# Kernel optimization log

Measured on AMD Instinct MI355X. Metric: run time of the kernel, lower is better.

The kernel has to match this reference:

```python
import jax, jax.numpy as jnp
import numpy as np

L = 2          # num_layers
D = 2048       # embed_dim
HQ = 16        # num_q_heads
HK = 4         # num_kv_heads
HD = D // HQ   # head_size = 128
G = HQ // HK   # q_to_kv_ratio = 4
P = 8192       # embed_dim_proj
V = 32000      # vocab_size
B = 1
S = 2048
EPS = 1e-5
THETA = 500000.0
NEG = -1e30


def setup_inputs() -> dict:
    key = jax.random.key(0)
    ks = jax.random.split(key, 8)
    s = 0.02
    return {
        "tokens": jax.random.randint(ks[0], (B, S), 0, V, dtype=jnp.int32),
        "embed": jax.random.normal(ks[1], (V, D), jnp.float32) * s,
        "attn_norm_w": jnp.ones((L, D), jnp.float32),
        "qkv_w": jax.random.normal(ks[2], (L, D, D + 2 * HK * HD), jnp.float32) * s,
        "attn_out_w": jax.random.normal(ks[3], (L, D, D), jnp.float32) * s,
        "mlp_norm_w": jnp.ones((L, D), jnp.float32),
        "mlp_in_w": jax.random.normal(ks[4], (L, D, 2 * P), jnp.float32) * s,
        "mlp_out_w": jax.random.normal(ks[5], (L, P, D), jnp.float32) * s,
        "final_norm_w": jnp.ones((D,), jnp.float32),
        "lm_head_w": jax.random.normal(ks[6], (D, V), jnp.float32) * s,
    }


def _rms(x, w):
    return w * (x * jax.lax.rsqrt(jnp.mean(x * x, axis=-1, keepdims=True) + EPS))


def _rope_cos_sin():
    inv = 1.0 / (THETA ** (jnp.arange(0, HD, 2, dtype=jnp.float32) / HD))  # [HD/2]
    ang = jnp.arange(S, dtype=jnp.float32)[:, None] * inv[None, :]         # [S, HD/2]
    return jnp.cos(ang), jnp.sin(ang)


def _rope(t, cos, sin):
    # t: [B,S,H,HD]; interleaved complex rotation on (even, odd) pairs
    x = t.reshape(t.shape[:-1] + (HD // 2, 2))
    x0, x1 = x[..., 0], x[..., 1]
    c = cos[None, :, None, :]
    sn = sin[None, :, None, :]
    out = jnp.stack([x0 * c - x1 * sn, x0 * sn + x1 * c], axis=-1)
    return out.reshape(t.shape)


def _layer(x, nw1, wqkv, wo, nw2, wi, wmo, cos, sin, mask):
    # attention block (pre-norm, residual)
    h = _rms(x, nw1)
    qkv = h @ wqkv
    q = qkv[..., :D].reshape(B, S, HQ, HD)
    k = qkv[..., D:D + HK * HD].reshape(B, S, HK, HD)
    v = qkv[..., D + HK * HD:].reshape(B, S, HK, HD)
    q = _rope(q, cos, sin)
    k = _rope(k, cos, sin)
    # GQA: repeat_interleave along head dim
    k = jnp.repeat(k, G, axis=2)
    v = jnp.repeat(v, G, axis=2)
    scores = jnp.einsum('bqhd,bkhd->bhqk', q, k) / np.float32(np.sqrt(HD))
    scores = jnp.where(mask, scores, NEG)
    attn = jax.nn.softmax(scores, axis=-1)
    o = jnp.einsum('bhqk,bkhd->bqhd', attn, v).reshape(B, S, D)
    x = x + o @ wo
    # SwiGLU block (pre-norm, residual)
    h = _rms(x, nw2)
    gu = h @ wi
    gate, up = gu[..., :P], gu[..., P:]
    x = x + (jax.nn.silu(gate) * up) @ wmo
    return x


def reference(tokens, embed, attn_norm_w, qkv_w, attn_out_w, mlp_norm_w,
              mlp_in_w, mlp_out_w, final_norm_w, lm_head_w):
    cos, sin = _rope_cos_sin()
    mask = jnp.tril(jnp.ones((S, S), dtype=bool))  # offset=0 prefill -> causal
    x = embed[tokens]  # [B,S,D]
    for i in range(L):
        x = _layer(x, attn_norm_w[i], qkv_w[i], attn_out_w[i],
                   mlp_norm_w[i], mlp_in_w[i], mlp_out_w[i], cos, sin, mask)
    return _rms(x, final_norm_w) @ lm_head_w  # [B,S,V]
```

## Files before the change

### kernel.cpp

```cpp
#include <hip/hip_runtime.h>
#include <math.h>

#define S_LEN 2048
#define DMODEL 2048
#define NHQ 16
#define NHK 4
#define HDIM 128
#define PDIM 8192
#define VOCAB 32000
#define NQKV 3072
#define EPSI 1e-5f

typedef unsigned short u16;
typedef unsigned int u32;
typedef __bf16 bf16x8 __attribute__((ext_vector_type(8)));
typedef float f32x4 __attribute__((ext_vector_type(4)));

__device__ __forceinline__ u16 f2bf(float f){
  u32 u = __builtin_bit_cast(u32, f);
  u += 0x7fffu + ((u >> 16) & 1u);
  return (u16)(u >> 16);
}
__device__ __forceinline__ float bf2f(u16 h){
  u32 u = ((u32)h) << 16;
  return __builtin_bit_cast(float, u);
}
__device__ __forceinline__ bf16x8 ld8(const u16* p){
  return __builtin_bit_cast(bf16x8, *(const uint4*)p);
}
__device__ __forceinline__ f32x4 mfma16(bf16x8 a, bf16x8 b, f32x4 c){
  return __builtin_amdgcn_mfma_f32_16x16x32_bf16(a, b, c, 0, 0, 0);
}

#define GLOAD_LDS16(gp, lp) __builtin_amdgcn_global_load_lds( \
    (__attribute__((address_space(1))) void*)(gp), \
    (__attribute__((address_space(3))) void*)(lp), 16, 0, 0)

__device__ __forceinline__ bf16x8 lds_frag(const u16* Lb, int R, int g){
  const int Rp = R >> 1;
  const int s8 = (((R & 1) << 2) | g) ^ (Rp & 7);
  return ld8(Lb + Rp * 64 + s8 * 8);
}
__device__ __forceinline__ void stage_sw(const u16* base, long row0, int K, int kt,
                                         int q, u16* Ldst_waveuniform){
  const int Rp = q >> 3;
  const int u = (q & 7) ^ (Rp & 7);
  const int R = (Rp << 1) | (u >> 2);
  const u16* gp = base + (row0 + R) * (long)K + kt + ((u & 3) << 3);
  GLOAD_LDS16(gp, Ldst_waveuniform);
}

__global__ void k_embed(const int* __restrict__ tok, const float* __restrict__ emb,
                        float* __restrict__ x){
  const int s = blockIdx.x, t = threadIdx.x;
  const long r = tok[s];
  const float4* src = (const float4*)(emb + r * DMODEL);
  float4* dst = (float4*)(x + (long)s * DMODEL);
  dst[t] = src[t];
  dst[t + 256] = src[t + 256];
}

__global__ void k_rmsnorm(const float* __restrict__ x, const float* __restrict__ w,
                          u16* __restrict__ out){
  const int s = blockIdx.x, t = threadIdx.x;
  const float4* xr = (const float4*)(x + (long)s * DMODEL);
  const float4 a = xr[t], b = xr[t + 256];
  float ss = a.x*a.x + a.y*a.y + a.z*a.z + a.w*a.w
           + b.x*b.x + b.y*b.y + b.z*b.z + b.w*b.w;
  #pragma unroll
  for (int off = 32; off > 0; off >>= 1) ss += __shfl_down(ss, off, 64);
  __shared__ float part[4];
  if ((t & 63) == 0) part[t >> 6] = ss;
  __syncthreads();
  const float r = rsqrtf((part[0] + part[1] + part[2] + part[3]) * (1.f / 2048.f) + EPSI);
  const float4* wr = (const float4*)w;
  const float4 wa = wr[t], wb = wr[t + 256];
  uint2 ua, ub;
  ua.x = (u32)f2bf(a.x*r*wa.x) | ((u32)f2bf(a.y*r*wa.y) << 16);
  ua.y = (u32)f2bf(a.z*r*wa.z) | ((u32)f2bf(a.w*r*wa.w) << 16);
  ub.x = (u32)f2bf(b.x*r*wb.x) | ((u32)f2bf(b.y*r*wb.y) << 16);
  ub.y = (u32)f2bf(b.z*r*wb.z) | ((u32)f2bf(b.w*r*wb.w) << 16);
  *(uint2*)(out + (long)s * DMODEL + 4 * t) = ua;
  *(uint2*)(out + (long)s * DMODEL + 1024 + 4 * t) = ub;
}

__global__ __launch_bounds__(256) void k_convT(const float* __restrict__ W,
                                               u16* __restrict__ Wt, int N, int K){
  const int n0 = blockIdx.x * 64, k0 = blockIdx.y * 64;
  const int t = threadIdx.x;
  __shared__ u16 T[64][72];
  const int r = t >> 4, c = (t & 15) << 2;
  #pragma unroll
  for (int p = 0; p < 4; ++p){
    const int k = p * 16 + r;
    const float4 v = *(const float4*)(W + (long)(k0 + k) * N + n0 + c);
    T[c + 0][k] = f2bf(v.x);
    T[c + 1][k] = f2bf(v.y);
    T[c + 2][k] = f2bf(v.z);
    T[c + 3][k] = f2bf(v.w);
  }
  __syncthreads();
  const int nr = t >> 3, kc = (t & 7) << 3;
  #pragma unroll
  for (int p = 0; p < 2; ++p){
    const int n = p * 32 + nr;
    *(uint4*)(Wt + (long)(n0 + n) * K + k0 + kc) = *(const uint4*)(&T[n][kc]);
  }
}

template<int OUT_BF16, int RES>
__global__ __launch_bounds__(256) void k_gemm(const u16* __restrict__ A, const u16* __restrict__ Bt,
                                              void* C, const float* Rs,
                                              int M, int N, int K){
  const int bm = blockIdx.x, bn = blockIdx.y;
  const int t = threadIdx.x;
  const int w = t >> 6, lane = t & 63, l15 = lane & 15, g = lane >> 4;
  const int wr = w >> 1, wc = w & 1;
  __shared__ u16 As[4096];
  __shared__ u16 Bs[4096];
  f32x4 acc[4][4] = {};
  const long arow = (long)bm * 128;
  const long brow = (long)bn * 128;
  for (int kt = 0; kt < K; kt += 32){
    __syncthreads();
    #pragma unroll
    for (int c = 0; c < 2; ++c){
      const int q0 = ((w << 1) | c) << 6;
      const int q  = q0 | lane;
      stage_sw(A,  arow, K, kt, q, As + q0 * 8);
      stage_sw(Bt, brow, K, kt, q, Bs + q0 * 8);
    }
    __syncthreads();
    bf16x8 af[4], bfr[4];
    #pragma unroll
    for (int i = 0; i < 4; ++i)
      af[i] = lds_frag(As, wr * 64 + i * 16 + l15, g);
    #pragma unroll
    for (int i = 0; i < 4; ++i)
      bfr[i] = lds_frag(Bs, wc * 64 + i * 16 + l15, g);
    #pragma unroll
    for (int mi = 0; mi < 4; ++mi)
      #pragma unroll
      for (int ni = 0; ni < 4; ++ni)
        acc[mi][ni] = mfma16(af[mi], bfr[ni], acc[mi][ni]);
  }
  const int row0 = bm * 128 + wr * 64, col0 = bn * 128 + wc * 64;
  #pragma unroll
  for (int mi = 0; mi < 4; ++mi){
    #pragma unroll
    for (int ni = 0; ni < 4; ++ni){
      #pragma unroll
      for (int r = 0; r < 4; ++r){
        const long ri = row0 + mi * 16 + g * 4 + r;
        const long ci = col0 + ni * 16 + l15;
        float v = acc[mi][ni][r];
        if (RES) v += Rs[ri * N + ci];
        if (OUT_BF16) ((u16*)C)[ri * N + ci] = f2bf(v);
        else          ((float*)C)[ri * N + ci] = v;
      }
    }
  }
}

template<int OUT_BF16>
__global__ __launch_bounds__(512, 2) void k_gemm256(const u16* __restrict__ A,
                                                    const u16* __restrict__ Bt,
                                                    void* C, int M, int N, int K){
  __shared__ u16 L[65536];
  const int t = threadIdx.x;
  const int w = t >> 6, lane = t & 63, l15 = lane & 15, g = lane >> 4;
  const int wr = w >> 2, wc = w & 3;
  const int nbm = M >> 8;
  int id = blockIdx.x;
  {
    const int cpx = gridDim.x >> 3;
    id = (id & 7) * cpx + (id >> 3);
  }
  const int bm = id % nbm, bn = id / nbm;
  const int NT = K >> 5;

  const int Rp0 = t >> 3;
  const int u0  = (t & 7) ^ (Rp0 & 7);
  const int R0  = (Rp0 << 1) | (u0 >> 2);
  const u16* pA0 = A  + ((long)bm * 256 + R0) * (long)K + ((u0 & 3) << 3);
  const u16* pB0 = Bt + ((long)bn * 256 + R0) * (long)K + ((u0 & 3) << 3);
  const u16* pA1 = pA0 + (long)128 * K;
  const u16* pB1 = pB0 + (long)128 * K;
  const int w0 = (t & ~63) * 8;

  auto stagef = [&](int slot){
    u16* ldsA = L + slot * 8192;
    u16* ldsB = L + 32768 + slot * 8192;
    GLOAD_LDS16(pA0, ldsA + w0);
    GLOAD_LDS16(pB0, ldsB + w0);
    GLOAD_LDS16(pA1, ldsA + 4096 + w0);
    GLOAD_LDS16(pB1, ldsB + 4096 + w0);
    pA0 += 32; pB0 += 32; pA1 += 32; pB1 += 32;
  };

  stagef(0); stagef(1); stagef(2);
  asm volatile("s_waitcnt vmcnt(8)" ::: "memory");
  __builtin_amdgcn_s_barrier();

  f32x4 acc[8][4] = {};
  for (int tt = 0; tt < NT; ++tt){
    const u16* sA = L + (tt & 3) * 8192;
    const u16* sB = L + 32768 + (tt & 3) * 8192;
    bf16x8 af[8], bfr[4];
    #pragma unroll
    for (int j = 0; j < 8; ++j)
      af[j] = lds_frag(sA, wr * 128 + j * 16 + l15, g);
    #pragma unroll
    for (int n = 0; n < 4; ++n)
      bfr[n] = lds_frag(sB, wc * 64 + n * 16 + l15, g);
    if (tt + 3 < NT) stagef((tt + 3) & 3);
    if (tt + 1 < NT){
      asm volatile("s_waitcnt lgkmcnt(0)" ::: "memory");
      if (tt + 3 < NT)      asm volatile("s_waitcnt vmcnt(8)" ::: "memory");
      else if (tt + 2 < NT) asm volatile("s_waitcnt vmcnt(4)" ::: "memory");
      else                  asm volatile("s_waitcnt vmcnt(0)" ::: "memory");
      __builtin_amdgcn_s_barrier();
    }
    __builtin_amdgcn_s_setprio(1);
    #pragma unroll
    for (int mi = 0; mi < 8; ++mi)
      #pragma unroll
      for (int ni = 0; ni < 4; ++ni)
        acc[mi][ni] = mfma16(af[mi], bfr[ni], acc[mi][ni]);
    __builtin_amdgcn_s_setprio(0);
  }
  const int row0 = bm * 256 + wr * 128, col0 = bn * 256 + wc * 64;
  #pragma unroll
  for (int mi = 0; mi < 8; ++mi){
    #pragma unroll
    for (int ni = 0; ni < 4; ++ni){
      #pragma unroll
      for (int r = 0; r < 4; ++r){
        const long ri = row0 + mi * 16 + g * 4 + r;
        const long ci = col0 + ni * 16 + l15;
        const float v = acc[mi][ni][r];
        if (OUT_BF16) ((u16*)C)[ri * N + ci] = f2bf(v);
        else          ((float*)C)[ri * N + ci] = v;
      }
    }
  }
}

__global__ void k_rope(u16* __restrict__ qkv){
  const int idx = blockIdx.x * 256 + threadIdx.x;
  const int i = idx & 63;
  const int head = (idx >> 6) % 20;
  const int s = idx / (64 * 20);
  const long base = (long)s * NQKV + (head < NHQ ? head * HDIM : DMODEL + (head - NHQ) * HDIM);
  u32* p = (u32*)(qkv + base + 2 * i);
  const u32 v = *p;
  const float x0 = bf2f((u16)(v & 0xffffu)), x1 = bf2f((u16)(v >> 16));
  const float ang = (float)s * exp2f(-0.29580575889569023f * (float)i);
  float sn, cs;
  sincosf(ang, &sn, &cs);
  const float y0 = x0 * cs - x1 * sn;
  const float y1 = x0 * sn + x1 * cs;
  *p = (u32)f2bf(y0) | ((u32)f2bf(y1) << 16);
}

__global__ __launch_bounds__(256) void k_attn(const u16* __restrict__ qkv, u16* __restrict__ o){
  const int qb = blockIdx.x, h = blockIdx.y;
  const int kh = h >> 2;
  const int t = threadIdx.x, w = t >> 6, lane = t & 63, l15 = lane & 15, g = lane >> 4;
  __shared__ u16 Ks[64 * 144];
  __shared__ u16 Vt[128 * 80];
  __shared__ u16 Ps[4][16 * 72];
  const int q0 = qb * 64 + w * 16;
  bf16x8 aq[4];
  #pragma unroll
  for (int d0 = 0; d0 < 4; ++d0)
    aq[d0] = ld8(qkv + (long)(q0 + l15) * NQKV + h * HDIM + d0 * 32 + g * 8);
  f32x4 acc_o[8] = {};
  float mst[4], lst[4];
  #pragma unroll
  for (int r = 0; r < 4; ++r){ mst[r] = -1e30f; lst[r] = 0.f; }
  const float scale = 0.08838834764831843f;
  const int krow = t >> 2, kc0 = (t & 3) << 5;
  const int vkv = (t & 31) << 1, vd0 = (t >> 5) << 4;
  for (int kt = 0; kt <= qb; ++kt){
    const int kv0 = kt << 6;
    __syncthreads();
    {
      const u16* kp = qkv + (long)(kv0 + krow) * NQKV + DMODEL + kh * HDIM + kc0;
      u16* kd = Ks + krow * 144 + kc0;
      #pragma unroll
      for (int c = 0; c < 4; ++c)
        *(uint4*)(kd + c * 8) = *(const uint4*)(kp + c * 8);
    }
    {
      const u16* vp = qkv + (long)(kv0 + vkv) * NQKV + DMODEL + 512 + kh * HDIM + vd0;
      const uint4 a0 = *(const uint4*)vp;
      const uint4 a1 = *(const uint4*)(vp + 8);
      const uint4 b0 = *(const uint4*)(vp + NQKV);
      const uint4 b1 = *(const uint4*)(vp + NQKV + 8);
      const u32 aw[8] = {a0.x,a0.y,a0.z,a0.w,a1.x,a1.y,a1.z,a1.w};
      const u32 bw[8] = {b0.x,b0.y,b0.z,b0.w,b1.x,b1.y,b1.z,b1.w};
      #pragma unroll
      for (int i2 = 0; i2 < 8; ++i2){
        *(u32*)(Vt + (vd0 + 2 * i2)     * 80 + vkv) = (aw[i2] & 0xffffu) | ((bw[i2] & 0xffffu) << 16);
        *(u32*)(Vt + (vd0 + 2 * i2 + 1) * 80 + vkv) = (aw[i2] >> 16)     | ((bw[i2] >> 16) << 16);
      }
    }
    __syncthreads();
    f32x4 sacc[4] = {};
    #pragma unroll
    for (int d0 = 0; d0 < 4; ++d0){
      #pragma unroll
      for (int j = 0; j < 4; ++j){
        const bf16x8 bk = ld8(Ks + (j * 16 + l15) * 144 + d0 * 32 + g * 8);
        sacc[j] = mfma16(aq[d0], bk, sacc[j]);
      }
    }
    float p[4][4], scl[4];
    #pragma unroll
    for (int r = 0; r < 4; ++r){
      const int qrow = q0 + g * 4 + r;
      float mx = -1e30f;
      #pragma unroll
      for (int j = 0; j < 4; ++j){
        float sv = sacc[j][r] * scale;
        sv = (kv0 + j * 16 + l15 <= qrow) ? sv : -1e30f;
        p[j][r] = sv;
        mx = fmaxf(mx, sv);
      }
      #pragma unroll
      for (int off = 1; off < 16; off <<= 1) mx = fmaxf(mx, __shfl_xor(mx, off, 64));
      const float mnew = fmaxf(mst[r], mx);
      scl[r] = __expf(mst[r] - mnew);
      float rs = 0.f;
      #pragma unroll
      for (int j = 0; j < 4; ++j){ p[j][r] = __expf(p[j][r] - mnew); rs += p[j][r]; }
      #pragma unroll
      for (int off = 1; off < 16; off <<= 1) rs += __shfl_xor(rs, off, 64);
      lst[r] = lst[r] * scl[r] + rs;
      mst[r] = mnew;
    }
    #pragma unroll
    for (int n = 0; n < 8; ++n)
      #pragma unroll
      for (int r = 0; r < 4; ++r)
        acc_o[n][r] *= scl[r];
    #pragma unroll
    for (int j = 0; j < 4; ++j)
      #pragma unroll
      for (int r = 0; r < 4; ++r)
        Ps[w][(g * 4 + r) * 72 + j * 16 + l15] = f2bf(p[j][r]);
    #pragma unroll
    for (int kk = 0; kk < 2; ++kk){
      const bf16x8 pa = ld8(Ps[w] + l15 * 72 + kk * 32 + g * 8);
      #pragma unroll
      for (int n = 0; n < 8; ++n){
        const bf16x8 bv = ld8(Vt + (n * 16 + l15) * 80 + kk * 32 + g * 8);
        acc_o[n] = mfma16(pa, bv, acc_o[n]);
      }
    }
  }
  #pragma unroll
  for (int n = 0; n < 8; ++n){
    #pragma unroll
    for (int r = 0; r < 4; ++r){
      const float ov = acc_o[n][r] / lst[r];
      o[(long)(q0 + g * 4 + r) * DMODEL + h * HDIM + n * 16 + l15] = f2bf(ov);
    }
  }
}

__global__ void k_swiglu(const u16* __restrict__ gu, u16* __restrict__ out){
  const long idx = ((long)blockIdx.x * 256 + threadIdx.x) * 8;
  const long s = idx >> 13;
  const int j = (int)(idx & 8191);
  const u16* gp = gu + s * 16384 + j;
  const uint4 gv = *(const uint4*)gp;
  const uint4 uv = *(const uint4*)(gp + PDIM);
  const u32 gw[4] = {gv.x, gv.y, gv.z, gv.w};
  const u32 uw[4] = {uv.x, uv.y, uv.z, uv.w};
  u32 ow[4];
  #pragma unroll
  for (int k = 0; k < 4; ++k){
    const float g0 = bf2f((u16)(gw[k] & 0xffffu)), g1 = bf2f((u16)(gw[k] >> 16));
    const float u0 = bf2f((u16)(uw[k] & 0xffffu)), u1 = bf2f((u16)(uw[k] >> 16));
    const float s0 = g0 / (1.f + __expf(-g0)) * u0;
    const float s1 = g1 / (1.f + __expf(-g1)) * u1;
    ow[k] = (u32)f2bf(s0) | ((u32)f2bf(s1) << 16);
  }
  uint4 ro; ro.x = ow[0]; ro.y = ow[1]; ro.z = ow[2]; ro.w = ow[3];
  *(uint4*)(out + idx) = ro;
}

extern "C" void kernel_launch(void* const* d_in, const int* in_sizes, int n_in,
                              void* d_out, int out_size, void* d_ws, size_t ws_size,
                              hipStream_t stream){
  const int*   tokens       = (const int*)d_in[0];
  const float* embed        = (const float*)d_in[1];
  const float* attn_norm_w  = (const float*)d_in[2];
  const float* qkv_w        = (const float*)d_in[3];
  const float* attn_out_w   = (const float*)d_in[4];
  const float* mlp_norm_w   = (const float*)d_in[5];
  const float* mlp_in_w     = (const float*)d_in[6];
  const float* mlp_out_w    = (const float*)d_in[7];
  const float* final_norm_w = (const float*)d_in[8];
  const float* lm_head_w    = (const float*)d_in[9];

  char* ws = (char*)d_ws;
  float* xf  = (float*)(ws);
  u16* hbf   = (u16*)(ws + 16777216);
  u16* qkvb  = (u16*)(ws + 25165824);
  u16* obf   = (u16*)(ws + 37748736);
  u16* gub   = (u16*)(ws + 46137344);
  u16* hb2   = (u16*)(ws + 113246208);
  u16* wbuf  = (u16*)(ws + 146800640);

  k_embed<<<S_LEN, 256, 0, stream>>>(tokens, embed, xf);
  for (int l = 0; l < 2; ++l){
    k_rmsnorm<<<S_LEN, 256, 0, stream>>>(xf, attn_norm_w + (long)l * DMODEL, hbf);
    k_convT<<<dim3(NQKV/64, DMODEL/64), 256, 0, stream>>>(
        qkv_w + (long)l * DMODEL * NQKV, wbuf, NQKV, DMODEL);
    k_gemm<1,0><<<dim3(S_LEN/128, NQKV/128), 256, 0, stream>>>(
        hbf, wbuf, qkvb, nullptr, S_LEN, NQKV, DMODEL);
    k_rope<<<(S_LEN * 20 * 64) / 256, 256, 0, stream>>>(qkvb);
    k_attn<<<dim3(S_LEN/64, NHQ), 256, 0, stream>>>(qkvb, obf);
    k_convT<<<dim3(DMODEL/64, DMODEL/64), 256, 0, stream>>>(
        attn_out_w + (long)l * DMODEL * DMODEL, wbuf, DMODEL, DMODEL);
    k_gemm<0,1><<<dim3(S_LEN/128, DMODEL/128), 256, 0, stream>>>(
        obf, wbuf, xf, xf, S_LEN, DMODEL, DMODEL);
    k_rmsnorm<<<S_LEN, 256, 0, stream>>>(xf, mlp_norm_w + (long)l * DMODEL, hbf);
    k_convT<<<dim3((2*PDIM)/64, DMODEL/64), 256, 0, stream>>>(
        mlp_in_w + (long)l * DMODEL * 2 * PDIM, wbuf, 2*PDIM, DMODEL);
    k_gemm256<1><<<(S_LEN/256) * ((2*PDIM)/256), 512, 0, stream>>>(
        hbf, wbuf, gub, S_LEN, 2*PDIM, DMODEL);
    k_swiglu<<<(S_LEN * PDIM / 8) / 256, 256, 0, stream>>>(gub, hb2);
    k_convT<<<dim3(DMODEL/64, PDIM/64), 256, 0, stream>>>(
        mlp_out_w + (long)l * PDIM * DMODEL, wbuf, DMODEL, PDIM);
    k_gemm<0,1><<<dim3(S_LEN/128, DMODEL/128), 256, 0, stream>>>(
        hb2, wbuf, xf, xf, S_LEN, DMODEL, PDIM);
  }
  k_rmsnorm<<<S_LEN, 256, 0, stream>>>(xf, final_norm_w, hbf);
  k_convT<<<dim3(VOCAB/64, DMODEL/64), 256, 0, stream>>>(lm_head_w, wbuf, VOCAB, DMODEL);
  k_gemm256<0><<<(S_LEN/256) * (VOCAB/256), 512, 0, stream>>>(
      hbf, wbuf, (float*)d_out, S_LEN, VOCAB, DMODEL);
}
```

Baseline: 1.602 ms.

## Double-buffer attention K/V via async LDS loads and split GEMM256 main loop

Adds a kernel that pre-transposes V into a separate buffer so the attention kernel can stage K and the transposed V with direct global-to-LDS loads into double-buffered, XOR-swizzled shared memory. The next tile's loads overlap with the current tile's compute, replacing the old synchronous per-tile register loads and scalar transposes. The 256-tile GEMM main loop is also split into two halves, interleaving A- and B-stage issue and fragment loads with MFMA work across two barriers. This costs an extra kernel launch, more workspace, and a second barrier per GEMM iteration.

```diff
diff --git a/kernel.cpp b/kernel.cpp
--- a/kernel.cpp
+++ b/kernel.cpp
@@ -105,6 +105,30 @@
   for (int p = 0; p < 2; ++p){
     const int n = p * 32 + nr;
     *(uint4*)(Wt + (long)(n0 + n) * K + k0 + kc) = *(const uint4*)(&T[n][kc]);
+  }
+}
+
+__global__ __launch_bounds__(256) void k_transV(const u16* __restrict__ qkv,
+                                                u16* __restrict__ vT){
+  const int s0 = blockIdx.x * 64, d0 = blockIdx.y * 64, kh = blockIdx.z;
+  const int t = threadIdx.x;
+  __shared__ u16 T[64][72];
+  #pragma unroll
+  for (int p = 0; p < 4; ++p){
+    const int s = p * 16 + (t >> 4);
+    const int c = (t & 15) * 4;
+    const uint2 v = *(const uint2*)(qkv + (long)(s0 + s) * NQKV + DMODEL + 512 + kh * HDIM + d0 + c);
+    T[c + 0][s] = (u16)(v.x);
+    T[c + 1][s] = (u16)(v.x >> 16);
+    T[c + 2][s] = (u16)(v.y);
+    T[c + 3][s] = (u16)(v.y >> 16);
+  }
+  __syncthreads();
+  #pragma unroll
+  for (int p = 0; p < 2; ++p){
+    const int d = p * 32 + (t >> 3);
+    *(uint4*)(vT + ((long)kh * HDIM + d0 + d) * S_LEN + s0 + (t & 7) * 8) =
+        *(const uint4*)(&T[d][(t & 7) * 8]);
   }
 }
 
@@ -188,17 +212,21 @@
   const u16* pB1 = pB0 + (long)128 * K;
   const int w0 = (t & ~63) * 8;
 
-  auto stagef = [&](int slot){
+  auto stageA = [&](int slot){
     u16* ldsA = L + slot * 8192;
+    GLOAD_LDS16(pA0, ldsA + w0);
+    GLOAD_LDS16(pA1, ldsA + 4096 + w0);
+    pA0 += 32; pA1 += 32;
+  };
+  auto stageB = [&](int slot){
     u16* ldsB = L + 32768 + slot * 8192;
-    GLOAD_LDS16(pA0, ldsA + w0);
     GLOAD_LDS16(pB0, ldsB + w0);
-    GLOAD_LDS16(pA1, ldsA + 4096 + w0);
     GLOAD_LDS16(pB1, ldsB + 4096 + w0);
-    pA0 += 32; pB0 += 32; pA1 += 32; pB1 += 32;
+    pB0 += 32; pB1 += 32;
   };
 
-  stagef(0); stagef(1); stagef(2);
+  #pragma unroll
+  for (int i = 0; i < 3; ++i){ stageA(i); stageB(i); }
   asm volatile("s_waitcnt vmcnt(8)" ::: "memory");
   __builtin_amdgcn_s_barrier();
 
@@ -206,27 +234,41 @@
   for (int tt = 0; tt < NT; ++tt){
     const u16* sA = L + (tt & 3) * 8192;
     const u16* sB = L + 32768 + (tt & 3) * 8192;
-    bf16x8 af[8], bfr[4];
-    #pragma unroll
-    for (int j = 0; j < 8; ++j)
-      af[j] = lds_frag(sA, wr * 128 + j * 16 + l15, g);
+    bf16x8 af0[4], bfr[4];
+    #pragma unroll
+    for (int j = 0; j < 4; ++j)
+      af0[j] = lds_frag(sA, wr * 128 + j * 16 + l15, g);
     #pragma unroll
     for (int n = 0; n < 4; ++n)
       bfr[n] = lds_frag(sB, wc * 64 + n * 16 + l15, g);
-    if (tt + 3 < NT) stagef((tt + 3) & 3);
+    if (tt + 3 < NT) stageA((tt + 3) & 3);
+    asm volatile("s_waitcnt lgkmcnt(0)" ::: "memory");
+    __builtin_amdgcn_s_barrier();
+    __builtin_amdgcn_s_setprio(1);
+    #pragma unroll
+    for (int mi = 0; mi < 4; ++mi)
+      #pragma unroll
+      for (int ni = 0; ni < 4; ++ni)
+        acc[mi][ni] = mfma16(af0[mi], bfr[ni], acc[mi][ni]);
+    __builtin_amdgcn_s_setprio(0);
+    bf16x8 af1[4];
+    #pragma unroll
+    for (int j = 0; j < 4; ++j)
+      af1[j] = lds_frag(sA, wr * 128 + 64 + j * 16 + l15, g);
+    if (tt + 3 < NT) stageB((tt + 3) & 3);
+    asm volatile("s_waitcnt lgkmcnt(0)" ::: "memory");
     if (tt + 1 < NT){
-      asm volatile("s_waitcnt lgkmcnt(0)" ::: "memory");
       if (tt + 3 < NT)      asm volatile("s_waitcnt vmcnt(8)" ::: "memory");
       else if (tt + 2 < NT) asm volatile("s_waitcnt vmcnt(4)" ::: "memory");
       else                  asm volatile("s_waitcnt vmcnt(0)" ::: "memory");
-      __builtin_amdgcn_s_barrier();
-    }
+    }
+    __builtin_amdgcn_s_barrier();
     __builtin_amdgcn_s_setprio(1);
     #pragma unroll
-    for (int mi = 0; mi < 8; ++mi)
+    for (int mi = 0; mi < 4; ++mi)
       #pragma unroll
       for (int ni = 0; ni < 4; ++ni)
-        acc[mi][ni] = mfma16(af[mi], bfr[ni], acc[mi][ni]);
+        acc[4 + mi][ni] = mfma16(af1[mi], bfr[ni], acc[4 + mi][ni]);
     __builtin_amdgcn_s_setprio(0);
   }
   const int row0 = bm * 256 + wr * 128, col0 = bn * 256 + wc * 64;
@@ -263,12 +305,14 @@
   *p = (u32)f2bf(y0) | ((u32)f2bf(y1) << 16);
 }
 
-__global__ __launch_bounds__(256) void k_attn(const u16* __restrict__ qkv, u16* __restrict__ o){
+__global__ __launch_bounds__(256) void k_attn(const u16* __restrict__ qkv,
+                                              const u16* __restrict__ vT,
+                                              u16* __restrict__ o){
   const int qb = blockIdx.x, h = blockIdx.y;
   const int kh = h >> 2;
   const int t = threadIdx.x, w = t >> 6, lane = t & 63, l15 = lane & 15, g = lane >> 4;
-  __shared__ u16 Ks[64 * 144];
-  __shared__ u16 Vt[128 * 80];
+  __shared__ u16 Ks[2][8192];
+  __shared__ u16 Vs[2][8192];
   __shared__ u16 Ps[4][16 * 72];
   const int q0 = qb * 64 + w * 16;
   bf16x8 aq[4];
@@ -280,39 +324,47 @@
   #pragma unroll
   for (int r = 0; r < 4; ++r){ mst[r] = -1e30f; lst[r] = 0.f; }
   const float scale = 0.08838834764831843f;
-  const int krow = t >> 2, kc0 = (t & 3) << 5;
-  const int vkv = (t & 31) << 1, vd0 = (t >> 5) << 4;
-  for (int kt = 0; kt <= qb; ++kt){
+
+  auto stageK = [&](int kt, int b){
+    #pragma unroll
+    for (int p = 0; p < 4; ++p){
+      const int q = p * 256 + t;
+      const int r = q >> 4, u = q & 15;
+      const u16* gp = qkv + (long)(kt * 64 + r) * NQKV + DMODEL + kh * HDIM + ((u ^ (r & 15)) << 3);
+      GLOAD_LDS16(gp, Ks[b] + (p * 256 + (t & ~63)) * 8);
+    }
+  };
+  auto stageV = [&](int kt, int b){
+    #pragma unroll
+    for (int p = 0; p < 4; ++p){
+      const int q = p * 256 + t;
+      const int r = q >> 3, u = q & 7;
+      const u16* gp = vT + ((long)kh * HDIM + r) * S_LEN + kt * 64 + ((u ^ (r & 7)) << 3);
+      GLOAD_LDS16(gp, Vs[b] + (p * 256 + (t & ~63)) * 8);
+    }
+  };
+
+  const int nkt = qb + 1;
+  stageK(0, 0); stageV(0, 0);
+  for (int kt = 0; kt < nkt; ++kt){
     const int kv0 = kt << 6;
-    __syncthreads();
-    {
-      const u16* kp = qkv + (long)(kv0 + krow) * NQKV + DMODEL + kh * HDIM + kc0;
-      u16* kd = Ks + krow * 144 + kc0;
-      #pragma unroll
-      for (int c = 0; c < 4; ++c)
-        *(uint4*)(kd + c * 8) = *(const uint4*)(kp + c * 8);
-    }
-    {
-      const u16* vp = qkv + (long)(kv0 + vkv) * NQKV + DMODEL + 512 + kh * HDIM + vd0;
-      const uint4 a0 = *(const uint4*)vp;
-      const uint4 a1 = *(const uint4*)(vp + 8);
-      const uint4 b0 = *(const uint4*)(vp + NQKV);
-      const uint4 b1 = *(const uint4*)(vp + NQKV + 8);
-      const u32 aw[8] = {a0.x,a0.y,a0.z,a0.w,a1.x,a1.y,a1.z,a1.w};
-      const u32 bw[8] = {b0.x,b0.y,b0.z,b0.w,b1.x,b1.y,b1.z,b1.w};
-      #pragma unroll
-      for (int i2 = 0; i2 < 8; ++i2){
-        *(u32*)(Vt + (vd0 + 2 * i2)     * 80 + vkv) = (aw[i2] & 0xffffu) | ((bw[i2] & 0xffffu) << 16);
-        *(u32*)(Vt + (vd0 + 2 * i2 + 1) * 80 + vkv) = (aw[i2] >> 16)     | ((bw[i2] >> 16) << 16);
-      }
-    }
-    __syncthreads();
+    __builtin_amdgcn_s_barrier();
+    if (kt + 1 < nkt){
+      stageK(kt + 1, (kt + 1) & 1);
+      stageV(kt + 1, (kt + 1) & 1);
+      asm volatile("s_waitcnt vmcnt(8)" ::: "memory");
+    } else {
+      asm volatile("s_waitcnt vmcnt(0)" ::: "memory");
+    }
+    __builtin_amdgcn_s_barrier();
+    const u16* K_ = Ks[kt & 1];
+    const u16* V_ = Vs[kt & 1];
     f32x4 sacc[4] = {};
     #pragma unroll
     for (int d0 = 0; d0 < 4; ++d0){
       #pragma unroll
       for (int j = 0; j < 4; ++j){
-        const bf16x8 bk = ld8(Ks + (j * 16 + l15) * 144 + d0 * 32 + g * 8);
+        const bf16x8 bk = ld8(K_ + (j * 16 + l15) * 128 + ((((d0 << 2) | g) ^ l15) << 3));
         sacc[j] = mfma16(aq[d0], bk, sacc[j]);
       }
     }
@@ -355,10 +407,12 @@
       const bf16x8 pa = ld8(Ps[w] + l15 * 72 + kk * 32 + g * 8);
       #pragma unroll
       for (int n = 0; n < 8; ++n){
-        const bf16x8 bv = ld8(Vt + (n * 16 + l15) * 80 + kk * 32 + g * 8);
+        const int row = n * 16 + l15;
+        const bf16x8 bv = ld8(V_ + row * 64 + ((((kk << 2) | g) ^ (l15 & 7)) << 3));
         acc_o[n] = mfma16(pa, bv, acc_o[n]);
       }
     }
+    asm volatile("s_waitcnt lgkmcnt(0)" ::: "memory");
   }
   #pragma unroll
   for (int n = 0; n < 8; ++n){
@@ -414,6 +468,7 @@
   u16* gub   = (u16*)(ws + 46137344);
   u16* hb2   = (u16*)(ws + 113246208);
   u16* wbuf  = (u16*)(ws + 146800640);
+  u16* vTb   = (u16*)(ws + 277872640);
 
   k_embed<<<S_LEN, 256, 0, stream>>>(tokens, embed, xf);
   for (int l = 0; l < 2; ++l){
@@ -423,7 +478,8 @@
     k_gemm<1,0><<<dim3(S_LEN/128, NQKV/128), 256, 0, stream>>>(
         hbf, wbuf, qkvb, nullptr, S_LEN, NQKV, DMODEL);
     k_rope<<<(S_LEN * 20 * 64) / 256, 256, 0, stream>>>(qkvb);
-    k_attn<<<dim3(S_LEN/64, NHQ), 256, 0, stream>>>(qkvb, obf);
+    k_transV<<<dim3(S_LEN/64, 2, 4), 256, 0, stream>>>(qkvb, vTb);
+    k_attn<<<dim3(S_LEN/64, NHQ), 256, 0, stream>>>(qkvb, vTb, obf);
     k_convT<<<dim3(DMODEL/64, DMODEL/64), 256, 0, stream>>>(
         attn_out_w + (long)l * DMODEL * DMODEL, wbuf, DMODEL, DMODEL);
     k_gemm<0,1><<<dim3(S_LEN/128, DMODEL/128), 256, 0, stream>>>(
```

Result: faster. 1.535 ms (-4.1%).
